# Optimization experiments

Measured on AMD Instinct MI355X. Metric: run time of the kernel, lower is better.

The kernel has to match this reference:

```python
import jax, jax.numpy as jnp
import numpy as np

B, S, H, E = 4, 2048, 1024, 8

def setup_inputs() -> dict:
    key = jax.random.key(0)
    k1, k2, k3 = jax.random.split(key, 3)
    scale_g = 1.0 / np.sqrt(H)
    scale_e = 1.0 / np.sqrt(H)
    return {
        "x": jax.random.normal(k1, (B, S, H), dtype=jnp.float32),
        "gate_w": jax.random.normal(k2, (H, E), dtype=jnp.float32) * scale_g,
        "gate_b": jnp.zeros((E,), dtype=jnp.float32),
        "expert_w": jax.random.normal(k3, (E, H, H), dtype=jnp.float32) * scale_e,
        "expert_b": jnp.zeros((E, H), dtype=jnp.float32),
    }

def reference(x, gate_w, gate_b, expert_w, expert_b):
    b, s, h = x.shape
    tok = x.reshape(-1, h)                                  # [T, H]
    # gate: softmax over experts per token
    w = jax.nn.softmax(tok @ gate_w + gate_b, axis=-1)      # [T, E]
    # all experts applied to all tokens (dense MoE)
    eo = jnp.einsum("th,ehd->ted", tok, expert_w) + expert_b[None]  # [T, E, H]
    out = jnp.einsum("te,ted->td", w, eo)                   # [T, H]
    return out.reshape(b, s, h)
```

## Files before the change

kernel.cpp:

```cpp
#include <hip/hip_runtime.h>
#include <stdint.h>

typedef unsigned short u16;
typedef short bf8 __attribute__((ext_vector_type(8)));
typedef float f4 __attribute__((ext_vector_type(4)));

#define TTOK 8192
#define HD   1024
#define NE   8

static __device__ __forceinline__ u16 f2bf(float f) {
  union { float f; uint32_t u; } v; v.f = f;
  return (u16)((v.u + 0x7fffu + ((v.u >> 16) & 1u)) >> 16);
}

__global__ __launch_bounds__(256) void gate_conv_kernel(
    const float* __restrict__ x, const float* __restrict__ gw,
    const float* __restrict__ gb, float* __restrict__ wout,
    u16* __restrict__ abf)
{
  const int t    = blockIdx.x * 4 + (threadIdx.x >> 6);
  const int lane = threadIdx.x & 63;
  const float* xr = x + (size_t)t * HD;
  float p[NE];
#pragma unroll
  for (int e = 0; e < NE; ++e) p[e] = 0.f;
#pragma unroll 4
  for (int h = lane; h < HD; h += 64) {
    const float xv = xr[h];
    abf[(size_t)t * HD + h] = f2bf(xv);
    const float* g = gw + (size_t)h * NE;
#pragma unroll
    for (int e = 0; e < NE; ++e) p[e] += xv * g[e];
  }
#pragma unroll
  for (int e = 0; e < NE; ++e) {
#pragma unroll
    for (int off = 32; off > 0; off >>= 1)
      p[e] += __shfl_xor(p[e], off, 64);
    p[e] += gb[e];
  }
  float m = p[0];
#pragma unroll
  for (int e = 1; e < NE; ++e) m = fmaxf(m, p[e]);
  float s = 0.f;
#pragma unroll
  for (int e = 0; e < NE; ++e) { p[e] = expf(p[e] - m); s += p[e]; }
  const float inv = 1.f / s;
  if (lane == 0) {
#pragma unroll
    for (int e = 0; e < NE; ++e) wout[t * NE + e] = p[e] * inv;
  }
}

__global__ __launch_bounds__(256) void wconv_kernel(
    const float* __restrict__ ew, u16* __restrict__ wt)
{
  __shared__ u16 tile[64][66];
  const int e  = blockIdx.z;
  const int h0 = blockIdx.y * 64;
  const int d0 = blockIdx.x * 64;
  const int c  = threadIdx.x & 63;
  const int r0 = threadIdx.x >> 6;
  const float* src = ew + (size_t)e * HD * HD;
  u16* dst = wt + (size_t)e * HD * HD;
#pragma unroll
  for (int i = 0; i < 16; ++i) {
    const int r = i * 4 + r0;
    tile[r][c] = f2bf(src[(size_t)(h0 + r) * HD + d0 + c]);
  }
  __syncthreads();
#pragma unroll
  for (int i = 0; i < 16; ++i) {
    const int r = i * 4 + r0;
    dst[(size_t)(d0 + r) * HD + h0 + c] = tile[c][r];
  }
}

#define BM 128
#define BN 128
#define BK 64

__global__ __launch_bounds__(256, 2) void moe_gemm_kernel(
    const u16* __restrict__ A,
    const u16* __restrict__ Wt,
    const float* __restrict__ wg,
    const float* __restrict__ eb,
    float* __restrict__ out)
{
  __shared__ u16 As[BM * BK];
  __shared__ u16 Bs[BN * BK];

  const int bid   = blockIdx.x;
  const int local = bid >> 3;
  const int bm    = (bid & 7) * 8 + (local & 7);
  const int bn    = local >> 3;

  const int tid  = threadIdx.x;
  const int lane = tid & 63;
  const int wid  = tid >> 6;
  const int wr   = wid >> 1;
  const int wc   = wid & 1;
  const int l15  = lane & 15;
  const int lhi  = lane >> 4;

  const int row0 = bm * BM;
  const int col0 = bn * BN;

  const f4 fz = {0.f, 0.f, 0.f, 0.f};
  f4 accO[4][4];
#pragma unroll
  for (int i = 0; i < 4; ++i)
#pragma unroll
    for (int j = 0; j < 4; ++j) accO[i][j] = fz;

  for (int e = 0; e < NE; ++e) {
    const u16* Bsrc = Wt + (size_t)e * HD * HD;
    f4 acc[4][4];
#pragma unroll
    for (int i = 0; i < 4; ++i)
#pragma unroll
      for (int j = 0; j < 4; ++j) acc[i][j] = fz;

    for (int kt = 0; kt < HD / BK; ++kt) {
      const int kcol = kt * BK;
#pragma unroll
      for (int j = 0; j < 4; ++j) {
        const int lin = j * 4096 + tid * 16;
        const int r   = lin >> 7;
        const int gsw = ((lin >> 4) & 7) ^ (r & 7);
        __builtin_amdgcn_global_load_lds(
            (const __attribute__((address_space(1))) void*)(A + (size_t)(row0 + r) * HD + kcol + gsw * 8),
            (__attribute__((address_space(3))) void*)((char*)As + lin),
            16, 0, 0);
        __builtin_amdgcn_global_load_lds(
            (const __attribute__((address_space(1))) void*)(Bsrc + (size_t)(col0 + r) * HD + kcol + gsw * 8),
            (__attribute__((address_space(3))) void*)((char*)Bs + lin),
            16, 0, 0);
      }
      __syncthreads();

#pragma unroll
      for (int kk = 0; kk < 2; ++kk) {
        bf8 af[4], bfr[4];
#pragma unroll
        for (int mi = 0; mi < 4; ++mi) {
          const int ar = wr * 64 + mi * 16 + l15;
          const int g  = kk * 4 + lhi;
          af[mi] = *(const bf8*)((const char*)As + ar * 128 + ((g ^ (ar & 7)) << 4));
        }
#pragma unroll
        for (int ni = 0; ni < 4; ++ni) {
          const int br = wc * 64 + ni * 16 + l15;
          const int g  = kk * 4 + lhi;
          bfr[ni] = *(const bf8*)((const char*)Bs + br * 128 + ((g ^ (br & 7)) << 4));
        }
#pragma unroll
        for (int mi = 0; mi < 4; ++mi)
#pragma unroll
          for (int ni = 0; ni < 4; ++ni)
            acc[mi][ni] = __builtin_amdgcn_mfma_f32_16x16x32_bf16(af[mi], bfr[ni], acc[mi][ni], 0, 0, 0);
      }
      __syncthreads();
    }

#pragma unroll
    for (int mi = 0; mi < 4; ++mi) {
      const int tb = row0 + wr * 64 + mi * 16 + lhi * 4;
      const float w0 = wg[(size_t)(tb + 0) * NE + e];
      const float w1 = wg[(size_t)(tb + 1) * NE + e];
      const float w2 = wg[(size_t)(tb + 2) * NE + e];
      const float w3 = wg[(size_t)(tb + 3) * NE + e];
#pragma unroll
      for (int ni = 0; ni < 4; ++ni) {
        accO[mi][ni][0] += w0 * acc[mi][ni][0];
        accO[mi][ni][1] += w1 * acc[mi][ni][1];
        accO[mi][ni][2] += w2 * acc[mi][ni][2];
        accO[mi][ni][3] += w3 * acc[mi][ni][3];
      }
    }
  }

#pragma unroll
  for (int mi = 0; mi < 4; ++mi) {
    const int tb = row0 + wr * 64 + mi * 16 + lhi * 4;
#pragma unroll
    for (int j = 0; j < 4; ++j) {
      const int t = tb + j;
#pragma unroll
      for (int ni = 0; ni < 4; ++ni) {
        const int d = col0 + wc * 64 + ni * 16 + l15;
        float bias = 0.f;
#pragma unroll
        for (int e2 = 0; e2 < NE; ++e2)
          bias += wg[(size_t)t * NE + e2] * eb[(size_t)e2 * HD + d];
        out[(size_t)t * HD + d] = accO[mi][ni][j] + bias;
      }
    }
  }
}

extern "C" void kernel_launch(void* const* d_in, const int* in_sizes, int n_in,
                              void* d_out, int out_size, void* d_ws, size_t ws_size,
                              hipStream_t stream) {
  const float* x  = (const float*)d_in[0];
  const float* gw = (const float*)d_in[1];
  const float* gb = (const float*)d_in[2];
  const float* ew = (const float*)d_in[3];
  const float* eb = (const float*)d_in[4];
  float* out = (float*)d_out;

  char* ws = (char*)d_ws;
  u16*   abf   = (u16*)ws;
  u16*   wt    = (u16*)(ws + (size_t)16 * 1024 * 1024);
  float* wgate = (float*)(ws + (size_t)32 * 1024 * 1024);

  gate_conv_kernel<<<dim3(TTOK / 4), dim3(256), 0, stream>>>(x, gw, gb, wgate, abf);
  wconv_kernel<<<dim3(16, 16, 8), dim3(256), 0, stream>>>(ew, wt);
  moe_gemm_kernel<<<dim3((TTOK / BM) * (HD / BN)), dim3(256), 0, stream>>>(abf, wt, wgate, eb, out);
}
```

Measured before the change: 167.8 us.

## Double-buffer MoE GEMM with 256x128 tiles, 8 waves and interleaved prefetch

The main GEMM now uses 256-row tiles with 512 threads (8 waves) and double-buffered LDS. The next K tile, including the one that crosses an expert boundary, is prefetched through global_load_lds while MFMAs run on the current buffer. Explicit s_barrier, sched_barrier and setprio calls schedule the MFMA phases, and the bias epilogue is restructured to preload expert biases and vector-load the gate weights. This is meant to hide global-load latency and cut per-tile synchronisation, at the cost of more LDS per block (96KB) and possibly lower occupancy.

```diff
diff --git a/kernel.cpp b/kernel.cpp
--- a/kernel.cpp
+++ b/kernel.cpp
@@ -77,24 +77,96 @@
   }
 }
 
-#define BM 128
+#define BM 256
 #define BN 128
 #define BK 64
 
-__global__ __launch_bounds__(256, 2) void moe_gemm_kernel(
+#define MM(a_, b_, c_) __builtin_amdgcn_mfma_f32_16x16x32_bf16((a_), (b_), (c_), 0, 0, 0)
+
+#define LDA(C, m, kk) (*(const bf8*)((const char*)As + (C) * 32768 + \
+    (wrb + (m) * 16 + l15) * 128 + ((((kk) * 4 + lhi) ^ (l15 & 7)) << 4)))
+#define LDB(C, n, kk) (*(const bf8*)((const char*)Bs + (C) * 16384 + \
+    (wcb + (n) * 16 + l15) * 128 + ((((kk) * 4 + lhi) ^ (l15 & 7)) << 4)))
+
+#define GLA(j) __builtin_amdgcn_global_load_lds( \
+    (const __attribute__((address_space(1))) void*)(aSrcT + (size_t)(j) * 65536), \
+    (__attribute__((address_space(3))) void*)(aDstT + (j) * 8192), 16, 0, 0)
+#define GLB(j) __builtin_amdgcn_global_load_lds( \
+    (const __attribute__((address_space(1))) void*)(bSrcT + (size_t)(j) * 65536), \
+    (__attribute__((address_space(3))) void*)(bDstT + (j) * 8192), 16, 0, 0)
+
+#define MFMA4(n_, b_) \
+    acc[0][n_] = MM(a0, (b_), acc[0][n_]); \
+    acc[1][n_] = MM(a1, (b_), acc[1][n_]); \
+    acc[2][n_] = MM(a2, (b_), acc[2][n_]); \
+    acc[3][n_] = MM(a3, (b_), acc[3][n_]);
+
+#define PRE_MFMA  __builtin_amdgcn_s_barrier(); \
+                  __builtin_amdgcn_sched_barrier(0); \
+                  __builtin_amdgcn_s_setprio(1);
+#define POST_MFMA __builtin_amdgcn_s_setprio(0); \
+                  __builtin_amdgcn_sched_barrier(0); \
+                  __builtin_amdgcn_s_barrier();
+
+#define TILE(qexpr, C)                                                          \
+  {                                                                             \
+    const int q_  = (qexpr);                                                    \
+    const int qn_ = (q_ < 127) ? (q_ + 1) : 127;                                \
+    const int en_ = qn_ >> 4;                                                   \
+    const int kcn_ = (qn_ & 15) << 6;                                           \
+    const u16* aSrcT = aSrc0 + kcn_;                                            \
+    const u16* bSrcT = bSrc0 + (size_t)en_ * (HD * HD) + kcn_;                  \
+    char* aDstT = aDstB + ((C) ^ 1) * 32768;                                    \
+    char* bDstT = bDstB + ((C) ^ 1) * 16384;                                    \
+    bf8 a0, a1, a2, a3, b0, b1;                                                 \
+                                                            \
+    a0 = LDA(C, 0, 0); a1 = LDA(C, 1, 0); a2 = LDA(C, 2, 0); a3 = LDA(C, 3, 0);  \
+    b0 = LDB(C, 0, 0); b1 = LDB(C, 1, 0);                                       \
+    GLA(0); GLA(1); GLB(0);                                                     \
+    PRE_MFMA                                                                    \
+    MFMA4(0, b0) MFMA4(1, b1)                                                   \
+    POST_MFMA                                                                   \
+                                                            \
+    b0 = LDB(C, 2, 0); b1 = LDB(C, 3, 0);                                       \
+    GLA(2); GLA(3); GLB(1);                                                     \
+    PRE_MFMA                                                                    \
+    MFMA4(2, b0) MFMA4(3, b1)                                                   \
+    POST_MFMA                                                                   \
+                                                            \
+    a0 = LDA(C, 0, 1); a1 = LDA(C, 1, 1); a2 = LDA(C, 2, 1); a3 = LDA(C, 3, 1);  \
+    b0 = LDB(C, 0, 1); b1 = LDB(C, 1, 1);                                       \
+    PRE_MFMA                                                                    \
+    MFMA4(0, b0) MFMA4(1, b1)                                                   \
+    POST_MFMA                                                                   \
+                                                            \
+    b0 = LDB(C, 2, 1); b1 = LDB(C, 3, 1);                                       \
+    __builtin_amdgcn_s_barrier();                                               \
+    __builtin_amdgcn_sched_barrier(0);                                          \
+    __builtin_amdgcn_s_setprio(1);                                              \
+    MFMA4(2, b0) MFMA4(3, b1)                                                   \
+    __builtin_amdgcn_s_setprio(0);                                              \
+    __builtin_amdgcn_sched_barrier(0);                                          \
+    asm volatile("s_waitcnt vmcnt(0)" ::: "memory");                            \
+    __builtin_amdgcn_s_barrier();                                               \
+  }
+
+__global__ __launch_bounds__(512, 2) void moe_gemm_kernel(
     const u16* __restrict__ A,
     const u16* __restrict__ Wt,
     const float* __restrict__ wg,
     const float* __restrict__ eb,
     float* __restrict__ out)
 {
-  __shared__ u16 As[BM * BK];
-  __shared__ u16 Bs[BN * BK];
+  __shared__ u16 As[2 * BM * BK];
+  __shared__ u16 Bs[2 * BN * BK];
 
   const int bid   = blockIdx.x;
+  const int xcd   = bid & 7;
   const int local = bid >> 3;
-  const int bm    = (bid & 7) * 8 + (local & 7);
-  const int bn    = local >> 3;
+  const int bm    = xcd * 4 + (local & 3);
+  const int bn    = local >> 2;
+  const int row0  = bm * BM;
+  const int col0  = bn * BN;
 
   const int tid  = threadIdx.x;
   const int lane = tid & 63;
@@ -103,70 +175,42 @@
   const int wc   = wid & 1;
   const int l15  = lane & 15;
   const int lhi  = lane >> 4;
-
-  const int row0 = bm * BM;
-  const int col0 = bn * BN;
+  const int wrb  = wr * 64;
+  const int wcb  = wc * 64;
+
+  const int row_in = tid >> 3;
+  const int gsw    = (tid & 7) ^ ((tid >> 3) & 7);
+  const u16* aSrc0 = A  + (size_t)(row0 + row_in) * HD + gsw * 8;
+  const u16* bSrc0 = Wt + (size_t)(col0 + row_in) * HD + gsw * 8;
+  char* aDstB = (char*)As + tid * 16;
+  char* bDstB = (char*)Bs + tid * 16;
 
   const f4 fz = {0.f, 0.f, 0.f, 0.f};
-  f4 accO[4][4];
+  f4 acc[4][4], accO[4][4];
 #pragma unroll
   for (int i = 0; i < 4; ++i)
 #pragma unroll
-    for (int j = 0; j < 4; ++j) accO[i][j] = fz;
+    for (int j = 0; j < 4; ++j) { acc[i][j] = fz; accO[i][j] = fz; }
+
+  {
+    const u16* aSrcT = aSrc0;
+    const u16* bSrcT = bSrc0;
+    char* aDstT = aDstB;
+    char* bDstT = bDstB;
+    GLA(0); GLA(1); GLA(2); GLA(3); GLB(0); GLB(1);
+  }
+  asm volatile("s_waitcnt vmcnt(0)" ::: "memory");
+  __builtin_amdgcn_s_barrier();
 
   for (int e = 0; e < NE; ++e) {
-    const u16* Bsrc = Wt + (size_t)e * HD * HD;
-    f4 acc[4][4];
-#pragma unroll
-    for (int i = 0; i < 4; ++i)
-#pragma unroll
-      for (int j = 0; j < 4; ++j) acc[i][j] = fz;
-
-    for (int kt = 0; kt < HD / BK; ++kt) {
-      const int kcol = kt * BK;
-#pragma unroll
-      for (int j = 0; j < 4; ++j) {
-        const int lin = j * 4096 + tid * 16;
-        const int r   = lin >> 7;
-        const int gsw = ((lin >> 4) & 7) ^ (r & 7);
-        __builtin_amdgcn_global_load_lds(
-            (const __attribute__((address_space(1))) void*)(A + (size_t)(row0 + r) * HD + kcol + gsw * 8),
-            (__attribute__((address_space(3))) void*)((char*)As + lin),
-            16, 0, 0);
-        __builtin_amdgcn_global_load_lds(
-            (const __attribute__((address_space(1))) void*)(Bsrc + (size_t)(col0 + r) * HD + kcol + gsw * 8),
-            (__attribute__((address_space(3))) void*)((char*)Bs + lin),
-            16, 0, 0);
-      }
-      __syncthreads();
-
-#pragma unroll
-      for (int kk = 0; kk < 2; ++kk) {
-        bf8 af[4], bfr[4];
-#pragma unroll
-        for (int mi = 0; mi < 4; ++mi) {
-          const int ar = wr * 64 + mi * 16 + l15;
-          const int g  = kk * 4 + lhi;
-          af[mi] = *(const bf8*)((const char*)As + ar * 128 + ((g ^ (ar & 7)) << 4));
-        }
-#pragma unroll
-        for (int ni = 0; ni < 4; ++ni) {
-          const int br = wc * 64 + ni * 16 + l15;
-          const int g  = kk * 4 + lhi;
-          bfr[ni] = *(const bf8*)((const char*)Bs + br * 128 + ((g ^ (br & 7)) << 4));
-        }
-#pragma unroll
-        for (int mi = 0; mi < 4; ++mi)
-#pragma unroll
-          for (int ni = 0; ni < 4; ++ni)
-            acc[mi][ni] = __builtin_amdgcn_mfma_f32_16x16x32_bf16(af[mi], bfr[ni], acc[mi][ni], 0, 0, 0);
-      }
-      __syncthreads();
+    for (int kt2 = 0; kt2 < 8; ++kt2) {
+      const int qb = e * 16 + kt2 * 2;
+      TILE(qb, 0)
+      TILE(qb + 1, 1)
     }
-
 #pragma unroll
     for (int mi = 0; mi < 4; ++mi) {
-      const int tb = row0 + wr * 64 + mi * 16 + lhi * 4;
+      const int tb = row0 + wrb + mi * 16 + lhi * 4;
       const float w0 = wg[(size_t)(tb + 0) * NE + e];
       const float w1 = wg[(size_t)(tb + 1) * NE + e];
       const float w2 = wg[(size_t)(tb + 2) * NE + e];
@@ -177,23 +221,34 @@
         accO[mi][ni][1] += w1 * acc[mi][ni][1];
         accO[mi][ni][2] += w2 * acc[mi][ni][2];
         accO[mi][ni][3] += w3 * acc[mi][ni][3];
+        acc[mi][ni] = fz;
       }
     }
   }
 
+  float ebv[4][8];
+#pragma unroll
+  for (int ni = 0; ni < 4; ++ni) {
+    const int d = col0 + wcb + ni * 16 + l15;
+#pragma unroll
+    for (int e2 = 0; e2 < NE; ++e2) ebv[ni][e2] = eb[(size_t)e2 * HD + d];
+  }
 #pragma unroll
   for (int mi = 0; mi < 4; ++mi) {
-    const int tb = row0 + wr * 64 + mi * 16 + lhi * 4;
+    const int tb = row0 + wrb + mi * 16 + lhi * 4;
 #pragma unroll
     for (int j = 0; j < 4; ++j) {
       const int t = tb + j;
+      const f4 wlo = *(const f4*)(wg + (size_t)t * NE);
+      const f4 whi = *(const f4*)(wg + (size_t)t * NE + 4);
 #pragma unroll
       for (int ni = 0; ni < 4; ++ni) {
-        const int d = col0 + wc * 64 + ni * 16 + l15;
-        float bias = 0.f;
-#pragma unroll
-        for (int e2 = 0; e2 < NE; ++e2)
-          bias += wg[(size_t)t * NE + e2] * eb[(size_t)e2 * HD + d];
+        const float bias =
+            wlo[0] * ebv[ni][0] + wlo[1] * ebv[ni][1] +
+            wlo[2] * ebv[ni][2] + wlo[3] * ebv[ni][3] +
+            whi[0] * ebv[ni][4] + whi[1] * ebv[ni][5] +
+            whi[2] * ebv[ni][6] + whi[3] * ebv[ni][7];
+        const int d = col0 + wcb + ni * 16 + l15;
         out[(size_t)t * HD + d] = accO[mi][ni][j] + bias;
       }
     }
@@ -217,5 +272,5 @@
 
   gate_conv_kernel<<<dim3(TTOK / 4), dim3(256), 0, stream>>>(x, gw, gb, wgate, abf);
   wconv_kernel<<<dim3(16, 16, 8), dim3(256), 0, stream>>>(ew, wt);
-  moe_gemm_kernel<<<dim3((TTOK / BM) * (HD / BN)), dim3(256), 0, stream>>>(abf, wt, wgate, eb, out);
-}
+  moe_gemm_kernel<<<dim3((TTOK / BM) * (HD / BN)), dim3(512), 0, stream>>>(abf, wt, wgate, eb, out);
+}
```

Measured after the change: 194.3 us. 15.8% more time.
